# Optimization experiments

Measured on AMD Instinct MI355X. Metric: run time of the kernel, lower is better.

Reference implementation:

```python
import jax, jax.numpy as jnp
import numpy as np
from jax.scipy.special import logsumexp

B, T = 32, 512
WV, CV = 32000, 8000
DW, DC = 128, 64
H = 128          # hidden per direction (hidden_size // 2)
L = 32           # num_labels


def setup_inputs() -> dict:
    key = jax.random.key(0)
    ks = jax.random.split(key, 16)
    D = DW + DC
    def n(k, shape, s=0.1):
        return jax.random.normal(k, shape, jnp.float32) * s
    return {
        'word': jax.random.randint(ks[0], (B, T), 1, WV),
        'char': jax.random.randint(ks[1], (B, T), 1, CV),  # >0 so mask is all ones
        'y': jax.random.randint(ks[2], (B, T), 0, L),
        'wordemb': n(ks[3], (WV, DW)),
        'charemb': n(ks[4], (CV, DC)),
        'W_ih_f': n(ks[5], (4 * H, D)), 'W_hh_f': n(ks[6], (4 * H, H)), 'b_f': n(ks[7], (4 * H,)),
        'W_ih_b': n(ks[8], (4 * H, D)), 'W_hh_b': n(ks[9], (4 * H, H)), 'b_b': n(ks[10], (4 * H,)),
        'W_out': n(ks[11], (L, 2 * H)), 'b_out': n(ks[12], (L,)),
        'trans': n(ks[13], (L, L)), 'start': n(ks[14], (L,)), 'end': n(ks[15], (L,)),
    }


def _lstm_scan(x_proj, W_hh):
    # x_proj: [T, B, 4H] = x @ W_ih.T + b, precomputed (batched GEMM)
    h0 = jnp.zeros((x_proj.shape[1], W_hh.shape[1]), x_proj.dtype)
    def step(carry, xt):
        h, c = carry
        g = xt + h @ W_hh.T                      # [B, 4H]
        i, f, gg, o = jnp.split(g, 4, axis=-1)   # PyTorch gate order i,f,g,o
        c = jax.nn.sigmoid(f) * c + jax.nn.sigmoid(i) * jnp.tanh(gg)
        h = jax.nn.sigmoid(o) * jnp.tanh(c)
        return (h, c), h
    _, hs = jax.lax.scan(step, (h0, h0), x_proj)
    return hs  # [T, B, H]


def reference(word, char, y, wordemb, charemb, W_ih_f, W_hh_f, b_f,
              W_ih_b, W_hh_b, b_b, W_out, b_out, trans, start, end):
    mask = (char > 0).astype(jnp.float32)                 # [B, T]
    x = jnp.concatenate([wordemb[word], charemb[char]], axis=-1)  # [B, T, D]

    # BiLSTM
    xp_f = (jnp.einsum('btd,gd->tbg', x, W_ih_f) + b_f)   # [T, B, 4H]
    xp_b = (jnp.einsum('btd,gd->tbg', x, W_ih_b) + b_b)[::-1]
    h_f = _lstm_scan(xp_f, W_hh_f)                        # [T, B, H]
    h_b = _lstm_scan(xp_b, W_hh_b)[::-1]                  # [T, B, H]
    h = jnp.concatenate([h_f, h_b], axis=-1).transpose(1, 0, 2)  # [B, T, 2H]

    emit = (jnp.einsum('bth,lh->btl', h, W_out) + b_out) * mask[:, :, None]  # [B, T, L]

    # CRF log-partition (forward algorithm)
    alpha0 = start + emit[:, 0]                           # [B, L]
    def crf_step(alpha, inp):
        e_t, m_t = inp                                    # [B, L], [B]
        new = logsumexp(alpha[:, :, None] + trans, axis=1) + e_t
        alpha = jnp.where(m_t[:, None] > 0, new, alpha)
        return alpha, None
    alpha, _ = jax.lax.scan(crf_step, alpha0,
                            (emit.transpose(1, 0, 2)[1:], mask.T[1:]))
    logZ = logsumexp(alpha + end, axis=-1)                # [B]

    # gold path score
    emit_score = (jnp.take_along_axis(emit, y[:, :, None], axis=-1)[..., 0] * mask).sum(1)
    trans_score = (trans[y[:, :-1], y[:, 1:]] * mask[:, 1:]).sum(1)
    last = mask.sum(1).astype(jnp.int32) - 1
    y_last = y[jnp.arange(y.shape[0]), last]
    gold = start[y[:, 0]] + emit_score + trans_score + end[y_last]

    return jnp.sum(logZ - gold)  # NLL, summed over batch
```

## Files before the change

kernel.cpp:

```cpp
#include <hip/hip_runtime.h>
#include <math.h>

#define BB 32
#define TT 512
#define DW 128
#define DC 64
#define DD 192
#define HH 128
#define G4 512
#define LL 32

typedef __fp16 h2_t __attribute__((ext_vector_type(2)));

__device__ __forceinline__ h2_t bch2(unsigned int x) { return __builtin_bit_cast(h2_t, x); }

__device__ __forceinline__ float qxor1(float x) {
    return __int_as_float(__builtin_amdgcn_update_dpp(0, __float_as_int(x), 0xB1, 0xF, 0xF, true));
}
__device__ __forceinline__ float qxor2(float x) {
    return __int_as_float(__builtin_amdgcn_update_dpp(0, __float_as_int(x), 0x4E, 0xF, 0xF, true));
}
__device__ __forceinline__ float qbcast(float x, int ctrl_imm) {
    switch (ctrl_imm) {
        case 0: return __int_as_float(__builtin_amdgcn_update_dpp(0, __float_as_int(x), 0x00, 0xF, 0xF, true));
        case 1: return __int_as_float(__builtin_amdgcn_update_dpp(0, __float_as_int(x), 0x55, 0xF, 0xF, true));
        case 2: return __int_as_float(__builtin_amdgcn_update_dpp(0, __float_as_int(x), 0xAA, 0xF, 0xF, true));
        default:return __int_as_float(__builtin_amdgcn_update_dpp(0, __float_as_int(x), 0xFF, 0xF, 0xF, true));
    }
}

__global__ __launch_bounds__(512) void k_inproj(
    const int* __restrict__ word, const int* __restrict__ charr,
    const float* __restrict__ wemb, const float* __restrict__ cemb,
    const float* __restrict__ Wf, const float* __restrict__ bf,
    const float* __restrict__ Wb, const float* __restrict__ bb,
    float* __restrict__ xpf, float* __restrict__ xpb)
{
    __shared__ __align__(16) h2_t As2[96][132];
    __shared__ __align__(16) h2_t Bs2[96][260];
    const int tid = threadIdx.x;
    const int ntile = blockIdx.x;
    const int ctile = blockIdx.y;
    const int dir = ctile >> 1;
    const float* W = dir ? Wb : Wf;
    const float* bias = dir ? bb : bf;
    float* xp = dir ? xpb : xpf;
    const int colbase = (ctile & 1) * 256;

    {
        const int lrow = tid >> 2;
        const int lq   = tid & 3;
        const int nA   = ntile * 128 + lrow;
        const int wi   = word[nA];
        const int ci   = charr[nA];
#pragma unroll
        for (int kc = 0; kc < 12; ++kc) {
            const int k0 = kc * 16 + lq * 4;
            float4 av;
            if (k0 < DW) av = *(const float4*)(wemb + (size_t)wi * DW + k0);
            else         av = *(const float4*)(cemb + (size_t)ci * DC + (k0 - DW));
            const int kp = k0 >> 1;
            As2[kp    ][lrow] = __builtin_amdgcn_cvt_pkrtz(av.x, av.y);
            As2[kp + 1][lrow] = __builtin_amdgcn_cvt_pkrtz(av.z, av.w);
        }
    }
    {
        const int lcol = tid >> 1;
        const int lh   = tid & 1;
        const int g    = colbase + lcol;
#pragma unroll
        for (int kc = 0; kc < 24; ++kc) {
            const int k0 = kc * 8 + lh * 4;
            const float4 bv = *(const float4*)(W + (size_t)g * DD + k0);
            const int kp = k0 >> 1;
            Bs2[kp    ][lcol] = __builtin_amdgcn_cvt_pkrtz(bv.x, bv.y);
            Bs2[kp + 1][lcol] = __builtin_amdgcn_cvt_pkrtz(bv.z, bv.w);
        }
    }
    __syncthreads();

    const int tr = tid >> 5;
    const int tc = tid & 31;
    float acc[8][8];
#pragma unroll
    for (int i = 0; i < 8; ++i)
#pragma unroll
        for (int j = 0; j < 8; ++j) acc[i][j] = 0.f;

    for (int kc = 0; kc < 24; ++kc) {
#pragma unroll
        for (int kq = 0; kq < 4; ++kq) {
            const int kp = kc * 4 + kq;
            h2_t __attribute__((aligned(16))) a2[8], b2[8];
            *(uint4*)&a2[0] = *(const uint4*)&As2[kp][tr * 8];
            *(uint4*)&a2[4] = *(const uint4*)&As2[kp][tr * 8 + 4];
            *(uint4*)&b2[0] = *(const uint4*)&Bs2[kp][tc * 8];
            *(uint4*)&b2[4] = *(const uint4*)&Bs2[kp][tc * 8 + 4];
#pragma unroll
            for (int i = 0; i < 8; ++i)
#pragma unroll
                for (int j = 0; j < 8; ++j)
                    acc[i][j] = __builtin_amdgcn_fdot2(a2[i], b2[j], acc[i][j], false);
        }
    }
#pragma unroll
    for (int i = 0; i < 8; ++i) {
        const int n  = ntile * 128 + tr * 8 + i;
        const int b_ = n >> 9, t_ = n & 511;
        float* dst = xp + ((size_t)(t_ * BB + b_)) * G4 + colbase + tc * 8;
#pragma unroll
        for (int j = 0; j < 8; ++j) dst[j] = acc[i][j] + bias[colbase + tc * 8 + j];
    }
}

__global__ __launch_bounds__(512)
__attribute__((amdgpu_waves_per_eu(2, 2)))
void k_lstm(
    const float* __restrict__ xpf, const float* __restrict__ xpb,
    const float* __restrict__ Whf, const float* __restrict__ Whb,
    float* __restrict__ hf, float* __restrict__ hb)
{
    __shared__ __align__(16) __fp16 hsd[2][160];
    const int tid = threadIdx.x;
    const int dir = blockIdx.x >> 5;
    const int b_  = blockIdx.x & 31;
    const float* xp = dir ? xpb : xpf;
    const float* Wh = dir ? Whb : Whf;
    float* hout = dir ? hb : hf;
    const int ks = tid & 3;
    const int u  = tid >> 2;

    h2_t w2[4][16];
#pragma unroll
    for (int g = 0; g < 4; ++g) {
        const float2* wp = (const float2*)(Wh + (size_t)(g * 128 + u) * HH + ks * 32);
#pragma unroll
        for (int j = 0; j < 16; ++j)
            w2[g][j] = __builtin_amdgcn_cvt_pkrtz(wp[j].x, wp[j].y);
    }

    const float mk0 = (ks == 0) ? 1.f : 0.f;
    const float mk1 = (ks == 1) ? 1.f : 0.f;
    const float mk2 = (ks == 2) ? 1.f : 0.f;
    const float mk3 = (ks == 3) ? 1.f : 0.f;
    const bool istanh = (ks == 2);
    const float GS  = istanh ? 2.f : -1.f;
    const float GC0 = istanh ? 1.f : 0.f;
    const float GC1 = istanh ? -2.f : 1.f;
    const bool ks1 = (ks & 1) != 0;
    const bool ks2 = (ks & 2) != 0;

    if (tid < 80) ((unsigned int*)&hsd[0][0])[tid] = 0u;
    float c = 0.f;
    const int t0 = dir ? (TT - 1) : 0;
    const int tstep = dir ? -1 : 1;
    const int xstride = tstep * BB * G4;
    const int hstride = tstep * BB * HH;
    const float* xqp = xp + ((long long)t0 * BB + b_) * G4 + ks * 128 + u;
    float*       hop = hout + ((long long)t0 * BB + b_) * HH + u;
    float xq = *xqp;
    __syncthreads();

    for (int s = 0; s < TT; ++s) {
        const int rb = s & 1;
        float p0 = mk0 * xq, p1 = mk1 * xq, p2 = mk2 * xq, p3 = mk3 * xq;
        xqp += xstride;
        xq = *xqp;
#pragma unroll
        for (int q = 0; q < 4; ++q) {
            const uint4 hv = *(const uint4*)&hsd[rb][ks * 40 + q * 8];
            const h2_t ha  = bch2(hv.x);
            const h2_t hbv = bch2(hv.y);
            const h2_t hc  = bch2(hv.z);
            const h2_t hd  = bch2(hv.w);
            p0 = __builtin_amdgcn_fdot2(ha,  w2[0][q*4+0], p0, false);
            p0 = __builtin_amdgcn_fdot2(hbv, w2[0][q*4+1], p0, false);
            p0 = __builtin_amdgcn_fdot2(hc,  w2[0][q*4+2], p0, false);
            p0 = __builtin_amdgcn_fdot2(hd,  w2[0][q*4+3], p0, false);
            p1 = __builtin_amdgcn_fdot2(ha,  w2[1][q*4+0], p1, false);
            p1 = __builtin_amdgcn_fdot2(hbv, w2[1][q*4+1], p1, false);
            p1 = __builtin_amdgcn_fdot2(hc,  w2[1][q*4+2], p1, false);
            p1 = __builtin_amdgcn_fdot2(hd,  w2[1][q*4+3], p1, false);
            p2 = __builtin_amdgcn_fdot2(ha,  w2[2][q*4+0], p2, false);
            p2 = __builtin_amdgcn_fdot2(hbv, w2[2][q*4+1], p2, false);
            p2 = __builtin_amdgcn_fdot2(hc,  w2[2][q*4+2], p2, false);
            p2 = __builtin_amdgcn_fdot2(hd,  w2[2][q*4+3], p2, false);
            p3 = __builtin_amdgcn_fdot2(ha,  w2[3][q*4+0], p3, false);
            p3 = __builtin_amdgcn_fdot2(hbv, w2[3][q*4+1], p3, false);
            p3 = __builtin_amdgcn_fdot2(hc,  w2[3][q*4+2], p3, false);
            p3 = __builtin_amdgcn_fdot2(hd,  w2[3][q*4+3], p3, false);
        }
        p0 += qxor1(p0); p0 += qxor2(p0);
        p1 += qxor1(p1); p1 += qxor2(p1);
        p2 += qxor1(p2); p2 += qxor2(p2);
        p3 += qxor1(p3); p3 += qxor2(p3);
        const float pa   = ks1 ? p1 : p0;
        const float pb   = ks1 ? p3 : p2;
        const float psel = ks2 ? pb : pa;
        const float val  = GC0 + GC1 * __builtin_amdgcn_rcpf(1.f + __expf(GS * psel));
        const float gi = qbcast(val, 0);
        const float gf = qbcast(val, 1);
        const float gg = qbcast(val, 2);
        const float go = qbcast(val, 3);
        c = gf * c + gi * gg;
        const float tc = 1.f - 2.f * __builtin_amdgcn_rcpf(1.f + __expf(2.f * c));
        const float hv = go * tc;
        if (ks == 0) {
            hsd[rb ^ 1][(u >> 5) * 40 + (u & 31)] = (__fp16)hv;
            *hop = hv;
        }
        hop += hstride;
        __builtin_amdgcn_sched_barrier(0);
        asm volatile("s_waitcnt lgkmcnt(0)");
        __builtin_amdgcn_s_barrier();
        __builtin_amdgcn_sched_barrier(0);
    }
}

__global__ __launch_bounds__(1024) void k_emit(
    const float* __restrict__ hf, const float* __restrict__ hb,
    const float* __restrict__ Wout, const float* __restrict__ bout,
    const int* __restrict__ charr, float* __restrict__ emit)
{
    __shared__ __align__(16) float hsm[BB * 256];
    __shared__ __align__(16) float wsm[LL * 260];
    const int t = blockIdx.x;
    const int tid = threadIdx.x;
    for (int idx = tid; idx < BB * 256; idx += 1024) {
        const int b_ = idx >> 8, u = idx & 255;
        hsm[idx] = (u < HH) ? hf[((size_t)t * BB + b_) * HH + u]
                            : hb[((size_t)t * BB + b_) * HH + (u - HH)];
    }
    for (int idx = tid; idx < LL * 256; idx += 1024) {
        const int l = idx >> 8, u = idx & 255;
        wsm[l * 260 + u] = Wout[idx];
    }
    __syncthreads();
    const int b_ = tid >> 5, l = tid & 31;
    float acc = bout[l];
#pragma unroll 8
    for (int q = 0; q < 64; ++q) {
        const float4 h4 = *(const float4*)&hsm[b_ * 256 + q * 4];
        const float4 w4 = *(const float4*)&wsm[l * 260 + q * 4];
        acc += h4.x * w4.x + h4.y * w4.y + h4.z * w4.z + h4.w * w4.w;
    }
    const float m = (charr[b_ * TT + t] > 0) ? 1.f : 0.f;
    emit[((size_t)t * BB + b_) * LL + l] = acc * m;
}

__global__ __launch_bounds__(64) void k_crf(
    const float* __restrict__ emit, const int* __restrict__ charr,
    const float* __restrict__ trans, const float* __restrict__ startv,
    const float* __restrict__ endv, float* __restrict__ logZ)
{
    const int tid = threadIdx.x;
    const int b_ = blockIdx.x;
    const int j = tid & 31;
    float et[32];
#pragma unroll
    for (int i = 0; i < 32; ++i) et[i] = __expf(trans[i * LL + j]);

    const float a0 = startv[j] + emit[(size_t)b_ * LL + j];
    float M = a0;
    M = fmaxf(M, __shfl_xor(M, 16));
    M = fmaxf(M, __shfl_xor(M, 8));
    M = fmaxf(M, __shfl_xor(M, 4));
    M = fmaxf(M, __shfl_xor(M, 2));
    M = fmaxf(M, __shfl_xor(M, 1));
    float A = __expf(a0 - M);
    float logsc = M;

    float e_nx = emit[((size_t)1 * BB + b_) * LL + j];
    int   m_nx = charr[b_ * TT + 1];

    for (int t = 1; t < TT; ++t) {
        const float ee = __expf(e_nx);
        const int m_cur = m_nx;
        if (t + 1 < TT) {
            e_nx = emit[((size_t)(t + 1) * BB + b_) * LL + j];
            m_nx = charr[b_ * TT + t + 1];
        }
        float s0 = 0.f, s1 = 0.f, s2 = 0.f, s3 = 0.f;
#pragma unroll
        for (int i = 0; i < 32; i += 4) {
            s0 = fmaf(__int_as_float(__builtin_amdgcn_readlane(__float_as_int(A), i    )), et[i    ], s0);
            s1 = fmaf(__int_as_float(__builtin_amdgcn_readlane(__float_as_int(A), i + 1)), et[i + 1], s1);
            s2 = fmaf(__int_as_float(__builtin_amdgcn_readlane(__float_as_int(A), i + 2)), et[i + 2], s2);
            s3 = fmaf(__int_as_float(__builtin_amdgcn_readlane(__float_as_int(A), i + 3)), et[i + 3], s3);
        }
        const float Anew = ((s0 + s1) + (s2 + s3)) * ee;
        A = (m_cur > 0) ? Anew : A;
        if ((t & 7) == 0) {
            float S = A;
            S = fmaxf(S, __shfl_xor(S, 16));
            S = fmaxf(S, __shfl_xor(S, 8));
            S = fmaxf(S, __shfl_xor(S, 4));
            S = fmaxf(S, __shfl_xor(S, 2));
            S = fmaxf(S, __shfl_xor(S, 1));
            A *= __builtin_amdgcn_rcpf(S);
            logsc += __logf(S);
        }
    }
    const float z = __logf(A) + logsc + endv[j];
    float Mz = z;
    Mz = fmaxf(Mz, __shfl_xor(Mz, 16));
    Mz = fmaxf(Mz, __shfl_xor(Mz, 8));
    Mz = fmaxf(Mz, __shfl_xor(Mz, 4));
    Mz = fmaxf(Mz, __shfl_xor(Mz, 2));
    Mz = fmaxf(Mz, __shfl_xor(Mz, 1));
    float sz = __expf(z - Mz);
    sz += __shfl_xor(sz, 16);
    sz += __shfl_xor(sz, 8);
    sz += __shfl_xor(sz, 4);
    sz += __shfl_xor(sz, 2);
    sz += __shfl_xor(sz, 1);
    if (tid == 0) logZ[b_] = Mz + __logf(sz);
}

__global__ __launch_bounds__(1024) void k_gold(
    const float* __restrict__ emit, const int* __restrict__ charr,
    const int* __restrict__ y, const float* __restrict__ trans,
    const float* __restrict__ startv, const float* __restrict__ endv,
    const float* __restrict__ logZ, float* __restrict__ out)
{
    __shared__ float red[BB];
    const int tid = threadIdx.x;
    const int b_ = tid >> 5, l = tid & 31;
    float sc = 0.f;
    int ms = 0;
    for (int t = l; t < TT; t += 32) {
        const int yv = y[b_ * TT + t];
        const int m = (charr[b_ * TT + t] > 0);
        if (m) { sc += emit[((size_t)t * BB + b_) * LL + yv]; ms++; }
        if (t + 1 < TT) {
            const int mn = (charr[b_ * TT + t + 1] > 0);
            if (mn) sc += trans[yv * LL + y[b_ * TT + t + 1]];
        }
    }
#pragma unroll
    for (int o = 16; o; o >>= 1) {
        sc += __shfl_xor(sc, o);
        ms += __shfl_xor(ms, o);
    }
    if (l == 0) {
        int last = ms - 1;
        if (last < 0) last = 0;
        const float gold = startv[y[b_ * TT]] + sc + endv[y[b_ * TT + last]];
        red[b_] = logZ[b_] - gold;
    }
    __syncthreads();
    if (tid == 0) {
        float tot = 0.f;
#pragma unroll
        for (int i = 0; i < BB; ++i) tot += red[i];
        out[0] = tot;
    }
}

extern "C" void kernel_launch(void* const* d_in, const int* in_sizes, int n_in,
                              void* d_out, int out_size, void* d_ws, size_t ws_size,
                              hipStream_t stream) {
    (void)in_sizes; (void)n_in; (void)out_size; (void)ws_size;
    const int*   word  = (const int*)d_in[0];
    const int*   charr = (const int*)d_in[1];
    const int*   yv    = (const int*)d_in[2];
    const float* wemb  = (const float*)d_in[3];
    const float* cemb  = (const float*)d_in[4];
    const float* Wihf  = (const float*)d_in[5];
    const float* Whhf  = (const float*)d_in[6];
    const float* bf    = (const float*)d_in[7];
    const float* Wihb  = (const float*)d_in[8];
    const float* Whhb  = (const float*)d_in[9];
    const float* bb    = (const float*)d_in[10];
    const float* Wout  = (const float*)d_in[11];
    const float* bout  = (const float*)d_in[12];
    const float* trans = (const float*)d_in[13];
    const float* startv= (const float*)d_in[14];
    const float* endv  = (const float*)d_in[15];

    float* ws   = (float*)d_ws;
    float* xpf  = ws;
    float* xpb  = xpf + (size_t)TT * BB * G4;
    float* hf   = xpb + (size_t)TT * BB * G4;
    float* hb   = hf + (size_t)TT * BB * HH;
    float* emit = hb + (size_t)TT * BB * HH;
    float* logZ = emit + (size_t)TT * BB * LL;

    k_inproj<<<dim3(128, 4), 512, 0, stream>>>(word, charr, wemb, cemb,
                                               Wihf, bf, Wihb, bb, xpf, xpb);
    k_lstm<<<64, 512, 0, stream>>>(xpf, xpb, Whhf, Whhb, hf, hb);
    k_emit<<<TT, 1024, 0, stream>>>(hf, hb, Wout, bout, charr, emit);
    k_crf<<<32, 64, 0, stream>>>(emit, charr, trans, startv, endv, logZ);
    k_gold<<<1, 1024, 0, stream>>>(emit, charr, yv, trans, startv, endv, logZ,
                                   (float*)d_out);
}
```

Baseline: 507.6 us.

## Store LSTM hidden states in fp16, use fdot2 in emit, fuse gold into CRF

The LSTM now writes its hidden states as fp16, which halves that global traffic. The emission kernel reads the packed halves and computes with fdot2 against fp16-converted W_out. The gold-path scoring kernel is folded into the CRF kernel, which adds its per-batch result to the output with an atomic, and the output is zeroed at the start of the input projection. This drops one kernel launch and the logZ round trip, at the cost of fp16 rounding on the emission inputs and a non-deterministic atomic summation order.

```diff
diff --git a/kernel.cpp b/kernel.cpp
--- a/kernel.cpp
+++ b/kernel.cpp
@@ -34,13 +34,15 @@
     const float* __restrict__ wemb, const float* __restrict__ cemb,
     const float* __restrict__ Wf, const float* __restrict__ bf,
     const float* __restrict__ Wb, const float* __restrict__ bb,
-    float* __restrict__ xpf, float* __restrict__ xpb)
+    float* __restrict__ xpf, float* __restrict__ xpb,
+    float* __restrict__ out)
 {
     __shared__ __align__(16) h2_t As2[96][132];
     __shared__ __align__(16) h2_t Bs2[96][260];
     const int tid = threadIdx.x;
     const int ntile = blockIdx.x;
     const int ctile = blockIdx.y;
+    if (ntile == 0 && ctile == 0 && tid == 0) out[0] = 0.f;
     const int dir = ctile >> 1;
     const float* W = dir ? Wb : Wf;
     const float* bias = dir ? bb : bf;
@@ -118,7 +120,7 @@
 void k_lstm(
     const float* __restrict__ xpf, const float* __restrict__ xpb,
     const float* __restrict__ Whf, const float* __restrict__ Whb,
-    float* __restrict__ hf, float* __restrict__ hb)
+    __fp16* __restrict__ hf, __fp16* __restrict__ hb)
 {
     __shared__ __align__(16) __fp16 hsd[2][160];
     const int tid = threadIdx.x;
@@ -126,7 +128,7 @@
     const int b_  = blockIdx.x & 31;
     const float* xp = dir ? xpb : xpf;
     const float* Wh = dir ? Whb : Whf;
-    float* hout = dir ? hb : hf;
+    __fp16* hout = dir ? hb : hf;
     const int ks = tid & 3;
     const int u  = tid >> 2;
 
@@ -157,7 +159,7 @@
     const int xstride = tstep * BB * G4;
     const int hstride = tstep * BB * HH;
     const float* xqp = xp + ((long long)t0 * BB + b_) * G4 + ks * 128 + u;
-    float*       hop = hout + ((long long)t0 * BB + b_) * HH + u;
+    __fp16*      hop = hout + ((long long)t0 * BB + b_) * HH + u;
     float xq = *xqp;
     __syncthreads();
 
@@ -205,9 +207,10 @@
         c = gf * c + gi * gg;
         const float tc = 1.f - 2.f * __builtin_amdgcn_rcpf(1.f + __expf(2.f * c));
         const float hv = go * tc;
+        const __fp16 hv16 = (__fp16)hv;
         if (ks == 0) {
-            hsd[rb ^ 1][(u >> 5) * 40 + (u & 31)] = (__fp16)hv;
-            *hop = hv;
+            hsd[rb ^ 1][(u >> 5) * 40 + (u & 31)] = hv16;
+            *hop = hv16;
         }
         hop += hstride;
         __builtin_amdgcn_sched_barrier(0);
@@ -218,31 +221,41 @@
 }
 
 __global__ __launch_bounds__(1024) void k_emit(
-    const float* __restrict__ hf, const float* __restrict__ hb,
+    const __fp16* __restrict__ hf, const __fp16* __restrict__ hb,
     const float* __restrict__ Wout, const float* __restrict__ bout,
     const int* __restrict__ charr, float* __restrict__ emit)
 {
-    __shared__ __align__(16) float hsm[BB * 256];
-    __shared__ __align__(16) float wsm[LL * 260];
+    __shared__ __align__(16) unsigned int hsm2[BB * 132];
+    __shared__ __align__(16) unsigned int wsm2[LL * 130];
     const int t = blockIdx.x;
     const int tid = threadIdx.x;
-    for (int idx = tid; idx < BB * 256; idx += 1024) {
-        const int b_ = idx >> 8, u = idx & 255;
-        hsm[idx] = (u < HH) ? hf[((size_t)t * BB + b_) * HH + u]
-                            : hb[((size_t)t * BB + b_) * HH + (u - HH)];
-    }
-    for (int idx = tid; idx < LL * 256; idx += 1024) {
-        const int l = idx >> 8, u = idx & 255;
-        wsm[l * 260 + u] = Wout[idx];
+    const unsigned int* hfu = (const unsigned int*)hf;
+    const unsigned int* hbu = (const unsigned int*)hb;
+    for (int idx = tid; idx < BB * 128; idx += 1024) {
+        const int b_ = idx >> 7, k = idx & 127;
+        const unsigned int v = (k < 64)
+            ? hfu[((size_t)t * BB + b_) * 64 + k]
+            : hbu[((size_t)t * BB + b_) * 64 + (k - 64)];
+        hsm2[b_ * 132 + k] = v;
+    }
+    for (int idx = tid; idx < LL * 128; idx += 1024) {
+        const int l = idx >> 7, kp = idx & 127;
+        const float2 wv = ((const float2*)Wout)[l * 128 + kp];
+        wsm2[l * 130 + kp] = __builtin_bit_cast(unsigned int,
+            __builtin_amdgcn_cvt_pkrtz(wv.x, wv.y));
     }
     __syncthreads();
     const int b_ = tid >> 5, l = tid & 31;
     float acc = bout[l];
 #pragma unroll 8
-    for (int q = 0; q < 64; ++q) {
-        const float4 h4 = *(const float4*)&hsm[b_ * 256 + q * 4];
-        const float4 w4 = *(const float4*)&wsm[l * 260 + q * 4];
-        acc += h4.x * w4.x + h4.y * w4.y + h4.z * w4.z + h4.w * w4.w;
+    for (int q = 0; q < 32; ++q) {
+        const uint4 h4 = *(const uint4*)&hsm2[b_ * 132 + q * 4];
+        const uint2 wa = *(const uint2*)&wsm2[l * 130 + q * 4];
+        const uint2 wb = *(const uint2*)&wsm2[l * 130 + q * 4 + 2];
+        acc = __builtin_amdgcn_fdot2(bch2(h4.x), bch2(wa.x), acc, false);
+        acc = __builtin_amdgcn_fdot2(bch2(h4.y), bch2(wa.y), acc, false);
+        acc = __builtin_amdgcn_fdot2(bch2(h4.z), bch2(wb.x), acc, false);
+        acc = __builtin_amdgcn_fdot2(bch2(h4.w), bch2(wb.y), acc, false);
     }
     const float m = (charr[b_ * TT + t] > 0) ? 1.f : 0.f;
     emit[((size_t)t * BB + b_) * LL + l] = acc * m;
@@ -250,12 +263,31 @@
 
 __global__ __launch_bounds__(64) void k_crf(
     const float* __restrict__ emit, const int* __restrict__ charr,
-    const float* __restrict__ trans, const float* __restrict__ startv,
-    const float* __restrict__ endv, float* __restrict__ logZ)
+    const int* __restrict__ y, const float* __restrict__ trans,
+    const float* __restrict__ startv, const float* __restrict__ endv,
+    float* __restrict__ out)
 {
     const int tid = threadIdx.x;
     const int b_ = blockIdx.x;
     const int j = tid & 31;
+
+    float sc = 0.f;
+    int ms = 0;
+    for (int t = tid; t < TT; t += 64) {
+        const int yv = y[b_ * TT + t];
+        const int m = (charr[b_ * TT + t] > 0);
+        if (m) { sc += emit[((size_t)t * BB + b_) * LL + yv]; ms++; }
+        if (t + 1 < TT) {
+            const int mn = (charr[b_ * TT + t + 1] > 0);
+            if (mn) sc += trans[yv * LL + y[b_ * TT + t + 1]];
+        }
+    }
+#pragma unroll
+    for (int o = 32; o; o >>= 1) {
+        sc += __shfl_xor(sc, o);
+        ms += __shfl_xor(ms, o);
+    }
+
     float et[32];
 #pragma unroll
     for (int i = 0; i < 32; ++i) et[i] = __expf(trans[i * LL + j]);
@@ -314,46 +346,12 @@
     sz += __shfl_xor(sz, 4);
     sz += __shfl_xor(sz, 2);
     sz += __shfl_xor(sz, 1);
-    if (tid == 0) logZ[b_] = Mz + __logf(sz);
-}
-
-__global__ __launch_bounds__(1024) void k_gold(
-    const float* __restrict__ emit, const int* __restrict__ charr,
-    const int* __restrict__ y, const float* __restrict__ trans,
-    const float* __restrict__ startv, const float* __restrict__ endv,
-    const float* __restrict__ logZ, float* __restrict__ out)
-{
-    __shared__ float red[BB];
-    const int tid = threadIdx.x;
-    const int b_ = tid >> 5, l = tid & 31;
-    float sc = 0.f;
-    int ms = 0;
-    for (int t = l; t < TT; t += 32) {
-        const int yv = y[b_ * TT + t];
-        const int m = (charr[b_ * TT + t] > 0);
-        if (m) { sc += emit[((size_t)t * BB + b_) * LL + yv]; ms++; }
-        if (t + 1 < TT) {
-            const int mn = (charr[b_ * TT + t + 1] > 0);
-            if (mn) sc += trans[yv * LL + y[b_ * TT + t + 1]];
-        }
-    }
-#pragma unroll
-    for (int o = 16; o; o >>= 1) {
-        sc += __shfl_xor(sc, o);
-        ms += __shfl_xor(ms, o);
-    }
-    if (l == 0) {
+    if (tid == 0) {
+        const float logZ = Mz + __logf(sz);
         int last = ms - 1;
         if (last < 0) last = 0;
         const float gold = startv[y[b_ * TT]] + sc + endv[y[b_ * TT + last]];
-        red[b_] = logZ[b_] - gold;
-    }
-    __syncthreads();
-    if (tid == 0) {
-        float tot = 0.f;
-#pragma unroll
-        for (int i = 0; i < BB; ++i) tot += red[i];
-        out[0] = tot;
+        atomicAdd(out, logZ - gold);
     }
 }
 
@@ -378,19 +376,18 @@
     const float* startv= (const float*)d_in[14];
     const float* endv  = (const float*)d_in[15];
 
-    float* ws   = (float*)d_ws;
-    float* xpf  = ws;
-    float* xpb  = xpf + (size_t)TT * BB * G4;
-    float* hf   = xpb + (size_t)TT * BB * G4;
-    float* hb   = hf + (size_t)TT * BB * HH;
-    float* emit = hb + (size_t)TT * BB * HH;
-    float* logZ = emit + (size_t)TT * BB * LL;
+    float* ws    = (float*)d_ws;
+    float* xpf   = ws;
+    float* xpb   = xpf + (size_t)TT * BB * G4;
+    __fp16* hf16 = (__fp16*)(xpb + (size_t)TT * BB * G4);
+    __fp16* hb16 = hf16 + (size_t)TT * BB * HH;
+    float* emit  = (float*)(hb16 + (size_t)TT * BB * HH);
 
     k_inproj<<<dim3(128, 4), 512, 0, stream>>>(word, charr, wemb, cemb,
-                                               Wihf, bf, Wihb, bb, xpf, xpb);
-    k_lstm<<<64, 512, 0, stream>>>(xpf, xpb, Whhf, Whhb, hf, hb);
-    k_emit<<<TT, 1024, 0, stream>>>(hf, hb, Wout, bout, charr, emit);
-    k_crf<<<32, 64, 0, stream>>>(emit, charr, trans, startv, endv, logZ);
-    k_gold<<<1, 1024, 0, stream>>>(emit, charr, yv, trans, startv, endv, logZ,
-                                   (float*)d_out);
-}
+                                               Wihf, bf, Wihb, bb, xpf, xpb,
+                                               (float*)d_out);
+    k_lstm<<<64, 512, 0, stream>>>(xpf, xpb, Whhf, Whhb, hf16, hb16);
+    k_emit<<<TT, 1024, 0, stream>>>(hf16, hb16, Wout, bout, charr, emit);
+    k_crf<<<32, 64, 0, stream>>>(emit, charr, yv, trans, startv, endv,
+                                 (float*)d_out);
+}
```

Result: faster. 435.7 us, median of 2 (-14.2%).
